# Optimization experiments

Hardware: AMD Instinct MI355X
Metric: run time of the kernel (lower is better)

## Reference

```python
import jax, jax.numpy as jnp
import numpy as np

D = 64      # size_in
RANK = 4    # rank
N = 262144  # batch of samples


def setup_inputs() -> dict:
    key = jax.random.key(0)
    k1, k2, k3, k4, k5 = jax.random.split(key, 5)
    s1 = 1.0 / np.sqrt(D)        # torch Linear init bound for linear1 (in=D)
    s2 = 1.0 / np.sqrt(2 * D)    # bound for linear2 (in=2D)
    return {
        "t": jnp.zeros((1,), dtype=jnp.float32),
        "input_": jax.random.normal(k1, (N, 2 * D), dtype=jnp.float32),
        "W1": jax.random.uniform(k2, (2 * D, D), jnp.float32, -s1, s1),
        "b1": jax.random.uniform(k3, (2 * D,), jnp.float32, -s1, s1),
        "W2": jax.random.uniform(k4, (RANK * D, 2 * D), jnp.float32, -s2, s2),
        "b2": jax.random.uniform(k5, (RANK * D,), jnp.float32, -s2, s2),
    }


def reference(t, input_, W1, b1, W2, b2):
    # Per-sample scalar Hamiltonian H(inp) = sum_j (v . W[:, j])^2 where
    # W = tanh(linear2(tanh(linear1(x)))).reshape(D, RANK); the torch einsum
    # 'mij,mhj,mi,mh->m' factors as sum_j (sum_i W[i,j] v[i])^2.
    def H(inp):
        x, v = inp[:D], inp[D:]
        h = jnp.tanh(W1 @ x + b1)                       # [2D]
        Wm = jnp.tanh(W2 @ h + b2).reshape(D, RANK)     # [D, RANK]
        return jnp.sum((v @ Wm) ** 2)

    # batch_jacobian of a scalar-per-sample fn == per-sample gradient [N, 2D]
    g = jax.vmap(jax.grad(H))(input_)
    dx = g[:, :D]
    dv = -g[:, D:]
    return jnp.concatenate([dx, dv], axis=-1)
```

## Files before the change

### kernel.cpp

```cpp
#include <hip/hip_runtime.h>

#define DD    64
#define TWOD  128
#define RD    256
#define NT    3

typedef __attribute__((ext_vector_type(8))) short short8;
typedef __attribute__((ext_vector_type(4))) float float4v;
typedef __attribute__((ext_vector_type(4))) unsigned uint4v;
typedef unsigned long long ull;
typedef unsigned short ush;

__device__ __forceinline__ ush f2b(float f) {
    unsigned u = __builtin_bit_cast(unsigned, f);
    u += 0x7fffu + ((u >> 16) & 1u);
    return (ush)(u >> 16);
}
__device__ __forceinline__ float b2f(ush s) {
    unsigned u = ((unsigned)s) << 16;
    return __builtin_bit_cast(float, u);
}
__device__ __forceinline__ unsigned cvt_pk_bf16(float lo, float hi) {
    unsigned r;
    asm("v_cvt_pk_bf16_f32 %0, %1, %2" : "=v"(r) : "v"(lo), "v"(hi));
    return r;
}
__device__ __forceinline__ void store_pair(ush* p0, ush* p1, float lo, float hi) {
    unsigned pk = cvt_pk_bf16(lo, hi);
    *p0 = (ush)pk;
    *p1 = (ush)(pk >> 16);
}
__device__ __forceinline__ float ftanh(float x) {
    float e, r;
    asm("v_exp_f32 %0, %1" : "=v"(e) : "v"(x * 2.885390082f));
    asm("v_rcp_f32 %0, %1" : "=v"(r) : "v"(e + 1.0f));
    return __builtin_fmaf(-2.0f, r, 1.0f);
}
__device__ __forceinline__ void lds_fence() {
    asm volatile("s_waitcnt lgkmcnt(0)" ::: "memory");
}

__global__ void prep_weights(const float* __restrict__ W1, const float* __restrict__ W2,
                             ush* __restrict__ wa, ush* __restrict__ wd,
                             ush* __restrict__ wb, ush* __restrict__ wc) {
    int t = blockIdx.x * blockDim.x + threadIdx.x;
    if (t < 8192) {
        wa[t] = f2b(W1[t]);
        int c = t >> 7, r = t & 127;
        wd[t] = f2b(W1[r * 64 + c]);
    }
    if (t < 32768) {
        wb[t] = f2b(W2[t]);
        int c = t >> 8, k = t & 255;
        wc[t] = f2b(W2[k * 128 + c]);
    }
}

__global__ __launch_bounds__(64, 2) void geognn_kernel(
    const float* __restrict__ inp, const float* __restrict__ b1, const float* __restrict__ b2,
    const ush* __restrict__ wa, const ush* __restrict__ wd,
    const ush* __restrict__ wb, const ush* __restrict__ wc,
    float* __restrict__ out, long nrows) {

    __shared__ __align__(16) ush hd_s[NT][16 * 264];
    __shared__ ush v_s[NT][16][68];
    __shared__ float4v y_s[NT][16];

    const int  l   = threadIdx.x;
    const int  l15 = l & 15;
    const int  q   = l >> 4;
    long row0 = (long)blockIdx.x * (16 * NT);
    if (row0 + 16 * NT > nrows) row0 = nrows - 16 * NT;

#pragma unroll
    for (int t = 0; t < NT; ++t)
#pragma unroll
        for (int r = 0; r < 16; r += 2) {
            float v0 = inp[(row0 + t * 16 + r)     * TWOD + DD + l];
            float v1 = inp[(row0 + t * 16 + r + 1) * TWOD + DD + l];
            store_pair(&v_s[t][r][l], &v_s[t][r + 1][l], v0, v1);
        }

    short8 ax[NT][2];
#pragma unroll
    for (int t = 0; t < NT; ++t)
#pragma unroll
        for (int kb = 0; kb < 2; ++kb) {
            const float4v* p = (const float4v*)(inp + (row0 + t * 16 + l15) * TWOD + kb * 32 + q * 8);
            float4v f0 = p[0], f1 = p[1];
            uint4v pk = { cvt_pk_bf16(f0.x, f0.y), cvt_pk_bf16(f0.z, f0.w),
                          cvt_pk_bf16(f1.x, f1.y), cvt_pk_bf16(f1.z, f1.w) };
            ax[t][kb] = __builtin_bit_cast(short8, pk);
        }

    float b1v[8];
#pragma unroll
    for (int nb = 0; nb < 8; ++nb) b1v[nb] = b1[nb * 16 + l15];
    float b2v[16];
#pragma unroll
    for (int nb = 0; nb < 16; ++nb) b2v[nb] = b2[nb * 16 + l15];

    short8 aw[16];
#pragma unroll
    for (int h = 0; h < 16; ++h)
        aw[h] = *(const short8*)(wa + ((h >> 1) * 16 + l15) * DD + (h & 1) * 32 + q * 8);

    unsigned g1p[NT][16];
#pragma unroll
    for (int nb = 0; nb < 8; ++nb) {
        const int c = nb * 16 + l15;
#pragma unroll
        for (int t = 0; t < NT; ++t) {
            float4v acc = {0.f, 0.f, 0.f, 0.f};
            acc = __builtin_amdgcn_mfma_f32_16x16x32_bf16(ax[t][0], aw[nb * 2 + 0], acc, 0, 0, 0);
            acc = __builtin_amdgcn_mfma_f32_16x16x32_bf16(ax[t][1], aw[nb * 2 + 1], acc, 0, 0, 0);
#pragma unroll
            for (int i = 0; i < 4; i += 2) {
                float h0 = ftanh(acc[i]     + b1v[nb]);
                float h1 = ftanh(acc[i + 1] + b1v[nb]);
                store_pair(&hd_s[t][(q * 4 + i) * 136 + c],
                           &hd_s[t][(q * 4 + i + 1) * 136 + c], h0, h1);
                g1p[t][nb * 2 + (i >> 1)] = cvt_pk_bf16(1.f - h0 * h0, 1.f - h1 * h1);
            }
        }
    }

    short8 bwA[8], bwB[8];
#pragma unroll
    for (int h = 0; h < 8; ++h)
        bwA[h] = *(const short8*)(wb + ((h >> 2) * 16 + l15) * TWOD + (h & 3) * 32 + q * 8);

    lds_fence();

    short8 ha[NT][4];
#pragma unroll
    for (int t = 0; t < NT; ++t)
#pragma unroll
        for (int kb = 0; kb < 4; ++kb)
            ha[t][kb] = *(const short8*)(&hd_s[t][l15 * 136 + kb * 32 + q * 8]);

    lds_fence();

    float yp[NT][4] = {};
#pragma unroll
    for (int p = 0; p < 8; ++p) {
        short8* cur = (p & 1) ? bwB : bwA;
        short8* nxt = (p & 1) ? bwA : bwB;
        if (p < 7) {
#pragma unroll
            for (int h = 0; h < 8; ++h)
                nxt[h] = *(const short8*)(wb + (((p + 1) * 2 + (h >> 2)) * 16 + l15) * TWOD
                                          + (h & 3) * 32 + q * 8);
        }
#pragma unroll
        for (int s = 0; s < 2; ++s) {
            const int nb = p * 2 + s;
            const int n  = nb * 16 + l15;
            const int c4 = nb * 4 + (l15 >> 2);
#pragma unroll
            for (int t = 0; t < NT; ++t) {
                float4v acc = {0.f, 0.f, 0.f, 0.f};
#pragma unroll
                for (int kb = 0; kb < 4; ++kb)
                    acc = __builtin_amdgcn_mfma_f32_16x16x32_bf16(ha[t][kb], cur[s * 4 + kb], acc, 0, 0, 0);
                float u0 = ftanh(acc[0] + b2v[nb]);
                float u1 = ftanh(acc[1] + b2v[nb]);
                float u2 = ftanh(acc[2] + b2v[nb]);
                float u3 = ftanh(acc[3] + b2v[nb]);
                store_pair(&hd_s[t][(q * 4 + 0) * 264 + n], &hd_s[t][(q * 4 + 1) * 264 + n], u0, u1);
                store_pair(&hd_s[t][(q * 4 + 2) * 264 + n], &hd_s[t][(q * 4 + 3) * 264 + n], u2, u3);
                yp[t][0] += b2f(v_s[t][q * 4 + 0][c4]) * u0;
                yp[t][1] += b2f(v_s[t][q * 4 + 1][c4]) * u1;
                yp[t][2] += b2f(v_s[t][q * 4 + 2][c4]) * u2;
                yp[t][3] += b2f(v_s[t][q * 4 + 3][c4]) * u3;
            }
        }
    }

#pragma unroll
    for (int t = 0; t < NT; ++t)
#pragma unroll
        for (int i = 0; i < 4; ++i) {
            yp[t][i] += __shfl_xor(yp[t][i], 4, 64);
            yp[t][i] += __shfl_xor(yp[t][i], 8, 64);
        }
    if (l15 < 4) {
#pragma unroll
        for (int t = 0; t < NT; ++t)
#pragma unroll
            for (int i = 0; i < 4; ++i)
                ((float*)&y_s[t][q * 4 + i])[l15] = yp[t][i];
    }

    short8 cwA[8], cwB[8];
#pragma unroll
    for (int kb = 0; kb < 8; ++kb)
        cwA[kb] = *(const short8*)(wc + l15 * RD + kb * 32 + q * 8);

    lds_fence();

#pragma unroll
    for (int t = 0; t < NT; ++t)
#pragma unroll
        for (int r = 0; r < 16; ++r) {
            ull uu = *(const ull*)(&hd_s[t][r * 264 + 4 * l]);
            float4v y = y_s[t][r];
            float vv = b2f(v_s[t][r][l]);
            float u0 = b2f((ush)uu);
            float u1 = b2f((ush)(uu >> 16));
            float u2 = b2f((ush)(uu >> 32));
            float u3 = b2f((ush)(uu >> 48));
            float dvv = y.x * u0 + y.y * u1 + y.z * u2 + y.w * u3;
            out[(row0 + t * 16 + r) * TWOD + DD + l] = -2.0f * dvv;
            float t0 = 2.0f * y.x * vv * (1.0f - u0 * u0);
            float t1 = 2.0f * y.y * vv * (1.0f - u1 * u1);
            float t2 = 2.0f * y.z * vv * (1.0f - u2 * u2);
            float t3 = 2.0f * y.w * vv * (1.0f - u3 * u3);
            unsigned w0 = cvt_pk_bf16(t0, t1);
            unsigned w1 = cvt_pk_bf16(t2, t3);
            ull w = (ull)w0 | ((ull)w1 << 32);
            *(ull*)(&hd_s[t][r * 264 + 4 * l]) = w;
        }

    lds_fence();

    short8 da[NT][8];
#pragma unroll
    for (int t = 0; t < NT; ++t)
#pragma unroll
        for (int kb = 0; kb < 8; ++kb)
            da[t][kb] = *(const short8*)(&hd_s[t][l15 * 264 + kb * 32 + q * 8]);

    lds_fence();

#pragma unroll
    for (int nb = 0; nb < 8; ++nb) {
        short8* cur = (nb & 1) ? cwB : cwA;
        short8* nxt = (nb & 1) ? cwA : cwB;
        if (nb < 7) {
#pragma unroll
            for (int kb = 0; kb < 8; ++kb)
                nxt[kb] = *(const short8*)(wc + ((nb + 1) * 16 + l15) * RD + kb * 32 + q * 8);
        }
        const int c = nb * 16 + l15;
#pragma unroll
        for (int t = 0; t < NT; ++t) {
            float4v acc = {0.f, 0.f, 0.f, 0.f};
#pragma unroll
            for (int kb = 0; kb < 8; ++kb)
                acc = __builtin_amdgcn_mfma_f32_16x16x32_bf16(da[t][kb], cur[kb], acc, 0, 0, 0);
            unsigned glo = g1p[t][nb * 2 + 0], ghi = g1p[t][nb * 2 + 1];
            float d0 = acc[0] * b2f((ush)glo);
            float d1 = acc[1] * b2f((ush)(glo >> 16));
            float d2 = acc[2] * b2f((ush)ghi);
            float d3 = acc[3] * b2f((ush)(ghi >> 16));
            store_pair(&hd_s[t][(q * 4 + 0) * 136 + c], &hd_s[t][(q * 4 + 1) * 136 + c], d0, d1);
            store_pair(&hd_s[t][(q * 4 + 2) * 136 + c], &hd_s[t][(q * 4 + 3) * 136 + c], d2, d3);
        }
    }

    short8 dw[16];
#pragma unroll
    for (int h = 0; h < 16; ++h)
        dw[h] = *(const short8*)(wd + ((h >> 2) * 16 + l15) * TWOD + (h & 3) * 32 + q * 8);

    lds_fence();

    short8 dfa[NT][4];
#pragma unroll
    for (int t = 0; t < NT; ++t)
#pragma unroll
        for (int kb = 0; kb < 4; ++kb)
            dfa[t][kb] = *(const short8*)(&hd_s[t][l15 * 136 + kb * 32 + q * 8]);
#pragma unroll
    for (int t = 0; t < NT; ++t)
#pragma unroll
        for (int nb = 0; nb < 4; ++nb) {
            float4v acc = {0.f, 0.f, 0.f, 0.f};
#pragma unroll
            for (int kb = 0; kb < 4; ++kb)
                acc = __builtin_amdgcn_mfma_f32_16x16x32_bf16(dfa[t][kb], dw[nb * 4 + kb], acc, 0, 0, 0);
#pragma unroll
            for (int i = 0; i < 4; ++i)
                out[(row0 + t * 16 + q * 4 + i) * TWOD + nb * 16 + l15] = acc[i];
        }
}

extern "C" void kernel_launch(void* const* d_in, const int* in_sizes, int n_in,
                              void* d_out, int out_size, void* d_ws, size_t ws_size,
                              hipStream_t stream) {
    const float* inp = (const float*)d_in[1];
    const float* W1  = (const float*)d_in[2];
    const float* b1  = (const float*)d_in[3];
    const float* W2  = (const float*)d_in[4];
    const float* b2  = (const float*)d_in[5];

    ush* wa = (ush*)d_ws;
    ush* wd = wa + 8192;
    ush* wb = wd + 8192;
    ush* wc = wb + 32768;

    prep_weights<<<128, 256, 0, stream>>>(W1, W2, wa, wd, wb, wc);

    const long rows = in_sizes[1] / TWOD;
    const int  grid = (int)((rows + 16 * NT - 1) / (16 * NT));
    geognn_kernel<<<grid, 64, 0, stream>>>(inp, b1, b2, wa, wd, wb, wc,
                                           (float*)d_out, rows);
}
```

Before: 345.8 us.

## Cut register pressure: drop g1p cache, stream biases, partially unroll stage loops

The first-layer tanh-derivative cache (g1p) is dropped and recomputed as d*(1-h^2) from the bf16 hidden activations already held in the ha registers, after the W2^T backward matmul. Biases are loaded per step instead of being held in arrays, and the W1 fragments are double-buffered rather than all preloaded. Several stage loops become unroll-1 pairs, and launch bounds change from 2 to 1 block per SIMD so the compiler has more registers to work with. The aim is to avoid spills and lower VGPR use. The cost is loop overhead, extra global loads for biases, and possibly lower occupancy and less latency hiding.

```diff
diff --git a/kernel.cpp b/kernel.cpp
--- a/kernel.cpp
+++ b/kernel.cpp
@@ -56,7 +56,7 @@
     }
 }
 
-__global__ __launch_bounds__(64, 2) void geognn_kernel(
+__global__ __launch_bounds__(64, 1) void geognn_kernel(
     const float* __restrict__ inp, const float* __restrict__ b1, const float* __restrict__ b2,
     const ush* __restrict__ wa, const ush* __restrict__ wd,
     const ush* __restrict__ wb, const ush* __restrict__ wc,
@@ -72,14 +72,15 @@
     long row0 = (long)blockIdx.x * (16 * NT);
     if (row0 + 16 * NT > nrows) row0 = nrows - 16 * NT;
 
-#pragma unroll
-    for (int t = 0; t < NT; ++t)
-#pragma unroll
-        for (int r = 0; r < 16; r += 2) {
+#pragma unroll 1
+    for (int r = 0; r < 16; r += 2) {
+#pragma unroll
+        for (int t = 0; t < NT; ++t) {
             float v0 = inp[(row0 + t * 16 + r)     * TWOD + DD + l];
             float v1 = inp[(row0 + t * 16 + r + 1) * TWOD + DD + l];
             store_pair(&v_s[t][r][l], &v_s[t][r + 1][l], v0, v1);
         }
+    }
 
     short8 ax[NT][2];
 #pragma unroll
@@ -93,42 +94,42 @@
             ax[t][kb] = __builtin_bit_cast(short8, pk);
         }
 
-    float b1v[8];
-#pragma unroll
-    for (int nb = 0; nb < 8; ++nb) b1v[nb] = b1[nb * 16 + l15];
-    float b2v[16];
-#pragma unroll
-    for (int nb = 0; nb < 16; ++nb) b2v[nb] = b2[nb * 16 + l15];
-
-    short8 aw[16];
-#pragma unroll
-    for (int h = 0; h < 16; ++h)
-        aw[h] = *(const short8*)(wa + ((h >> 1) * 16 + l15) * DD + (h & 1) * 32 + q * 8);
-
-    unsigned g1p[NT][16];
-#pragma unroll
-    for (int nb = 0; nb < 8; ++nb) {
+    short8 awA[2], awB[2];
+#pragma unroll
+    for (int f = 0; f < 2; ++f)
+        awA[f] = *(const short8*)(wa + (0 * 16 + l15) * DD + f * 32 + q * 8);
+
+    auto g1step = [&](int nb, short8* cur, short8* nxt) {
+        if (nb < 7) {
+#pragma unroll
+            for (int f = 0; f < 2; ++f)
+                nxt[f] = *(const short8*)(wa + ((nb + 1) * 16 + l15) * DD + f * 32 + q * 8);
+        }
+        float bv = b1[nb * 16 + l15];
         const int c = nb * 16 + l15;
 #pragma unroll
         for (int t = 0; t < NT; ++t) {
             float4v acc = {0.f, 0.f, 0.f, 0.f};
-            acc = __builtin_amdgcn_mfma_f32_16x16x32_bf16(ax[t][0], aw[nb * 2 + 0], acc, 0, 0, 0);
-            acc = __builtin_amdgcn_mfma_f32_16x16x32_bf16(ax[t][1], aw[nb * 2 + 1], acc, 0, 0, 0);
-#pragma unroll
-            for (int i = 0; i < 4; i += 2) {
-                float h0 = ftanh(acc[i]     + b1v[nb]);
-                float h1 = ftanh(acc[i + 1] + b1v[nb]);
-                store_pair(&hd_s[t][(q * 4 + i) * 136 + c],
-                           &hd_s[t][(q * 4 + i + 1) * 136 + c], h0, h1);
-                g1p[t][nb * 2 + (i >> 1)] = cvt_pk_bf16(1.f - h0 * h0, 1.f - h1 * h1);
-            }
-        }
+            acc = __builtin_amdgcn_mfma_f32_16x16x32_bf16(ax[t][0], cur[0], acc, 0, 0, 0);
+            acc = __builtin_amdgcn_mfma_f32_16x16x32_bf16(ax[t][1], cur[1], acc, 0, 0, 0);
+            float h0 = ftanh(acc[0] + bv);
+            float h1 = ftanh(acc[1] + bv);
+            float h2 = ftanh(acc[2] + bv);
+            float h3 = ftanh(acc[3] + bv);
+            store_pair(&hd_s[t][(q * 4 + 0) * 136 + c], &hd_s[t][(q * 4 + 1) * 136 + c], h0, h1);
+            store_pair(&hd_s[t][(q * 4 + 2) * 136 + c], &hd_s[t][(q * 4 + 3) * 136 + c], h2, h3);
+        }
+    };
+#pragma unroll 1
+    for (int nbb = 0; nbb < 8; nbb += 2) {
+        g1step(nbb,     awA, awB);
+        g1step(nbb + 1, awB, awA);
     }
 
     short8 bwA[8], bwB[8];
 #pragma unroll
-    for (int h = 0; h < 8; ++h)
-        bwA[h] = *(const short8*)(wb + ((h >> 2) * 16 + l15) * TWOD + (h & 3) * 32 + q * 8);
+    for (int f = 0; f < 8; ++f)
+        bwA[f] = *(const short8*)(wb + ((f >> 2) * 16 + l15) * TWOD + (f & 3) * 32 + q * 8);
 
     lds_fence();
 
@@ -142,31 +143,29 @@
     lds_fence();
 
     float yp[NT][4] = {};
-#pragma unroll
-    for (int p = 0; p < 8; ++p) {
-        short8* cur = (p & 1) ? bwB : bwA;
-        short8* nxt = (p & 1) ? bwA : bwB;
+    auto g2step = [&](int p, short8* cur, short8* nxt) {
         if (p < 7) {
 #pragma unroll
-            for (int h = 0; h < 8; ++h)
-                nxt[h] = *(const short8*)(wb + (((p + 1) * 2 + (h >> 2)) * 16 + l15) * TWOD
-                                          + (h & 3) * 32 + q * 8);
+            for (int f = 0; f < 8; ++f)
+                nxt[f] = *(const short8*)(wb + (((p + 1) * 2 + (f >> 2)) * 16 + l15) * TWOD
+                                          + (f & 3) * 32 + q * 8);
         }
 #pragma unroll
         for (int s = 0; s < 2; ++s) {
             const int nb = p * 2 + s;
             const int n  = nb * 16 + l15;
             const int c4 = nb * 4 + (l15 >> 2);
+            float bv = b2[nb * 16 + l15];
 #pragma unroll
             for (int t = 0; t < NT; ++t) {
                 float4v acc = {0.f, 0.f, 0.f, 0.f};
 #pragma unroll
                 for (int kb = 0; kb < 4; ++kb)
                     acc = __builtin_amdgcn_mfma_f32_16x16x32_bf16(ha[t][kb], cur[s * 4 + kb], acc, 0, 0, 0);
-                float u0 = ftanh(acc[0] + b2v[nb]);
-                float u1 = ftanh(acc[1] + b2v[nb]);
-                float u2 = ftanh(acc[2] + b2v[nb]);
-                float u3 = ftanh(acc[3] + b2v[nb]);
+                float u0 = ftanh(acc[0] + bv);
+                float u1 = ftanh(acc[1] + bv);
+                float u2 = ftanh(acc[2] + bv);
+                float u3 = ftanh(acc[3] + bv);
                 store_pair(&hd_s[t][(q * 4 + 0) * 264 + n], &hd_s[t][(q * 4 + 1) * 264 + n], u0, u1);
                 store_pair(&hd_s[t][(q * 4 + 2) * 264 + n], &hd_s[t][(q * 4 + 3) * 264 + n], u2, u3);
                 yp[t][0] += b2f(v_s[t][q * 4 + 0][c4]) * u0;
@@ -175,6 +174,11 @@
                 yp[t][3] += b2f(v_s[t][q * 4 + 3][c4]) * u3;
             }
         }
+    };
+#pragma unroll 1
+    for (int pp = 0; pp < 8; pp += 2) {
+        g2step(pp,     bwA, bwB);
+        g2step(pp + 1, bwB, bwA);
     }
 
 #pragma unroll
@@ -199,10 +203,10 @@
 
     lds_fence();
 
-#pragma unroll
-    for (int t = 0; t < NT; ++t)
-#pragma unroll
-        for (int r = 0; r < 16; ++r) {
+#pragma unroll 1
+    for (int r = 0; r < 16; ++r) {
+#pragma unroll
+        for (int t = 0; t < NT; ++t) {
             ull uu = *(const ull*)(&hd_s[t][r * 264 + 4 * l]);
             float4v y = y_s[t][r];
             float vv = b2f(v_s[t][r][l]);
@@ -221,6 +225,7 @@
             ull w = (ull)w0 | ((ull)w1 << 32);
             *(ull*)(&hd_s[t][r * 264 + 4 * l]) = w;
         }
+    }
 
     lds_fence();
 
@@ -233,10 +238,7 @@
 
     lds_fence();
 
-#pragma unroll
-    for (int nb = 0; nb < 8; ++nb) {
-        short8* cur = (nb & 1) ? cwB : cwA;
-        short8* nxt = (nb & 1) ? cwA : cwB;
+    auto g3step = [&](int nb, short8* cur, short8* nxt) {
         if (nb < 7) {
 #pragma unroll
             for (int kb = 0; kb < 8; ++kb)
@@ -249,29 +251,42 @@
 #pragma unroll
             for (int kb = 0; kb < 8; ++kb)
                 acc = __builtin_amdgcn_mfma_f32_16x16x32_bf16(da[t][kb], cur[kb], acc, 0, 0, 0);
-            unsigned glo = g1p[t][nb * 2 + 0], ghi = g1p[t][nb * 2 + 1];
-            float d0 = acc[0] * b2f((ush)glo);
-            float d1 = acc[1] * b2f((ush)(glo >> 16));
-            float d2 = acc[2] * b2f((ush)ghi);
-            float d3 = acc[3] * b2f((ush)(ghi >> 16));
-            store_pair(&hd_s[t][(q * 4 + 0) * 136 + c], &hd_s[t][(q * 4 + 1) * 136 + c], d0, d1);
-            store_pair(&hd_s[t][(q * 4 + 2) * 136 + c], &hd_s[t][(q * 4 + 3) * 136 + c], d2, d3);
-        }
-    }
+            store_pair(&hd_s[t][(q * 4 + 0) * 136 + c], &hd_s[t][(q * 4 + 1) * 136 + c], acc[0], acc[1]);
+            store_pair(&hd_s[t][(q * 4 + 2) * 136 + c], &hd_s[t][(q * 4 + 3) * 136 + c], acc[2], acc[3]);
+        }
+    };
+#pragma unroll 1
+    for (int nbb = 0; nbb < 8; nbb += 2) {
+        g3step(nbb,     cwA, cwB);
+        g3step(nbb + 1, cwB, cwA);
+    }
+
+    lds_fence();
 
     short8 dw[16];
 #pragma unroll
-    for (int h = 0; h < 16; ++h)
-        dw[h] = *(const short8*)(wd + ((h >> 2) * 16 + l15) * TWOD + (h & 3) * 32 + q * 8);
-
-    lds_fence();
+    for (int f = 0; f < 16; ++f)
+        dw[f] = *(const short8*)(wd + ((f >> 2) * 16 + l15) * TWOD + (f & 3) * 32 + q * 8);
 
     short8 dfa[NT][4];
 #pragma unroll
     for (int t = 0; t < NT; ++t)
 #pragma unroll
-        for (int kb = 0; kb < 4; ++kb)
-            dfa[t][kb] = *(const short8*)(&hd_s[t][l15 * 136 + kb * 32 + q * 8]);
+        for (int kb = 0; kb < 4; ++kb) {
+            short8 raw = *(const short8*)(&hd_s[t][l15 * 136 + kb * 32 + q * 8]);
+            uint4v pk;
+#pragma unroll
+            for (int j = 0; j < 4; ++j) {
+                float h0 = b2f((ush)ha[t][kb][2 * j]);
+                float d0 = b2f((ush)raw[2 * j]);
+                float h1 = b2f((ush)ha[t][kb][2 * j + 1]);
+                float d1 = b2f((ush)raw[2 * j + 1]);
+                float a0 = __builtin_fmaf(-(d0 * h0), h0, d0);
+                float a1 = __builtin_fmaf(-(d1 * h1), h1, d1);
+                pk[j] = cvt_pk_bf16(a0, a1);
+            }
+            dfa[t][kb] = __builtin_bit_cast(short8, pk);
+        }
 #pragma unroll
     for (int t = 0; t < NT; ++t)
 #pragma unroll
```

After: 391.9 us. 13.3% more time.
